# Kernel optimization log

Hardware: AMD Instinct MI355X
Metric: run time of the kernel (lower is better)

The kernel has to match this reference:

```python
import jax, jax.numpy as jnp
import numpy as np

EPS = 1e-12

def gcn_layer(x, W, row, col, vals, n_nodes):
    # support = x @ W ; out = relu(spmm(adj, support)) with adj in COO form
    support = x @ W                                  # [N, out]
    msgs = vals[:, None] * support[col]              # [E, out] gather
    agg = jax.ops.segment_sum(msgs, row, num_segments=n_nodes)
    return jax.nn.relu(agg)

def l2norm(x):
    return x / jnp.maximum(jnp.linalg.norm(x, axis=1, keepdims=True), EPS)

def setup_inputs() -> dict:
    key = jax.random.key(0)
    ks = jax.random.split(key, 16)
    N, D, A, Da, E = 20000, 1000, 1000, 100, 160000
    inp = {
        'emb_sr': jax.random.normal(ks[0], (N, D), jnp.float32) * 0.02,
        'emb_tg': jax.random.normal(ks[1], (N, D), jnp.float32) * 0.02,
        'attr_weight_sr': jax.random.uniform(ks[2], (N, A), jnp.float32),
        'attr_weight_tg': jax.random.uniform(ks[3], (N, A), jnp.float32),
        'row_sr': jax.random.randint(ks[4], (E,), 0, N, jnp.int32),
        'col_sr': jax.random.randint(ks[5], (E,), 0, N, jnp.int32),
        'vals_sr': jax.random.uniform(ks[6], (E,), jnp.float32),
        'row_tg': jax.random.randint(ks[7], (E,), 0, N, jnp.int32),
        'col_tg': jax.random.randint(ks[8], (E,), 0, N, jnp.int32),
        'vals_tg': jax.random.uniform(ks[9], (E,), jnp.float32),
        'W_s0': jax.random.normal(ks[10], (D, D), jnp.float32) * (1.0 / np.sqrt(D)),
        'W_s1': jax.random.normal(ks[11], (D, D), jnp.float32) * (1.0 / np.sqrt(D)),
        'W_a11': jax.random.normal(ks[12], (A, Da), jnp.float32) * (1.0 / np.sqrt(A)),
        'W_a12': jax.random.normal(ks[13], (A, Da), jnp.float32) * (1.0 / np.sqrt(A)),
        'W_a2': jax.random.normal(ks[14], (Da, Da), jnp.float32) * (1.0 / np.sqrt(Da)),
    }
    return inp

def reference(emb_sr, emb_tg, attr_weight_sr, attr_weight_tg,
              row_sr, col_sr, vals_sr, row_tg, col_tg, vals_tg,
              W_s0, W_s1, W_a11, W_a12, W_a2):
    N = emb_sr.shape[0]
    M = emb_tg.shape[0]
    # structural branch: 2 shared GCN layers over each graph
    sr = emb_sr
    tg = emb_tg
    for W in (W_s0, W_s1):
        sr = gcn_layer(sr, W, row_sr, col_sr, vals_sr, N)
        tg = gcn_layer(tg, W, row_tg, col_tg, vals_tg, M)
    sr = l2norm(sr)
    tg = l2norm(tg)
    # attribute branch
    sr_a = gcn_layer(attr_weight_sr, W_a11, row_sr, col_sr, vals_sr, N)
    sr_a = gcn_layer(sr_a, W_a2, row_sr, col_sr, vals_sr, N)
    tg_a = gcn_layer(attr_weight_tg, W_a12, row_tg, col_tg, vals_tg, M)
    tg_a = gcn_layer(tg_a, W_a2, row_tg, col_tg, vals_tg, M)
    return (sr, tg, sr_a, tg_a)
```

## Files before the change

kernel.cpp:

```cpp
#include <hip/hip_runtime.h>

#define N_NODES 20000
#define D_IN    1000
#define E_EDGES 160000
#define DA      100

#define MPAD 20224
#define DP   1024
#define DAP  128
#define MBLK 157
#define NRB  1250
#define PEMAX (E_EDGES + 4 * N_NODES)

typedef __bf16 bf16x8 __attribute__((ext_vector_type(8)));
typedef float  f32x4  __attribute__((ext_vector_type(4)));
typedef short  short8v __attribute__((ext_vector_type(8)));

__device__ __forceinline__ short f2bf(float f) {
  __bf16 h = (__bf16)f;
  return *(short*)&h;
}
__device__ __forceinline__ float bf2f(short s) {
  return __uint_as_float(((unsigned)(unsigned short)s) << 16);
}

#define GLDS16(g, l) __builtin_amdgcn_global_load_lds( \
    (const __attribute__((address_space(1))) void*)(g), \
    (__attribute__((address_space(3))) void*)(l), 16, 0, 0)


__global__ void cvt_pad2_k(const float* __restrict__ s0, const float* __restrict__ s1,
                           int R, int C,
                           short* __restrict__ d0, short* __restrict__ d1, int Cp) {
  const float* src = blockIdx.z ? s1 : s0;
  short* dst = blockIdx.z ? d1 : d0;
  int r = blockIdx.y;
  int c0 = threadIdx.x * 4;
  short4 o = {0, 0, 0, 0};
  if (r < R) {
    if (c0 + 3 < C) {
      float4 v = *(const float4*)&src[(size_t)r * C + c0];
      o.x = f2bf(v.x); o.y = f2bf(v.y); o.z = f2bf(v.z); o.w = f2bf(v.w);
    } else {
#pragma unroll
      for (int j = 0; j < 4; ++j) {
        float v = (c0 + j < C) ? src[(size_t)r * C + c0 + j] : 0.f;
        ((short*)&o)[j] = f2bf(v);
      }
    }
  }
  *(short4*)&dst[(size_t)r * Cp + c0] = o;
}

__global__ void cvt_w_t2_k(const float* __restrict__ s0, const float* __restrict__ s1,
                           int K, int Nc,
                           short* __restrict__ d0, short* __restrict__ d1, int Kp) {
  const float* src = blockIdx.z ? s1 : s0;
  short* dst = blockIdx.z ? d1 : d0;
  int n = blockIdx.y;
  int k = blockIdx.x * blockDim.x + threadIdx.x;
  if (k >= Kp) return;
  float v = (k < K && n < Nc) ? src[(size_t)k * Nc + n] : 0.f;
  dst[(size_t)n * Kp + k] = f2bf(v);
}

__global__ void zero_int_k(int* p, int n) {
  int i = blockIdx.x * blockDim.x + threadIdx.x;
  if (i < n) p[i] = 0;
}


__global__ void hist2_k(const int* __restrict__ row0, const int* __restrict__ row1, int E,
                        int* __restrict__ deg0, int* __restrict__ deg1) {
  int e = blockIdx.x * blockDim.x + threadIdx.x;
  if (e < E) atomicAdd(&deg0[row0[e]], 1);
  else if (e < 2 * E) atomicAdd(&deg1[row1[e - E]], 1);
}

#define SCAN_T 1024
#define SCAN_C 20
__launch_bounds__(SCAN_T)
__global__ void scan_pad2_k(const int* __restrict__ dg0, const int* __restrict__ dg1, int n,
                            int* __restrict__ p0, int* __restrict__ p1) {
  const int* deg = blockIdx.x ? dg1 : dg0;
  int* poffs = blockIdx.x ? p1 : p0;
  __shared__ int lds[SCAN_T];
  int t = threadIdx.x;
  int base = t * SCAN_C;
  int v[SCAN_C];
  int s = 0;
#pragma unroll
  for (int i = 0; i < SCAN_C; ++i) {
    int idx = base + i;
    int x = (idx < n) ? ((deg[idx] + 3) & ~3) : 0;
    s += x;
    v[i] = s;
  }
  lds[t] = s;
  __syncthreads();
  for (int off = 1; off < SCAN_T; off <<= 1) {
    int add = (t >= off) ? lds[t - off] : 0;
    __syncthreads();
    lds[t] += add;
    __syncthreads();
  }
  int prefix = lds[t] - s;
#pragma unroll
  for (int i = 0; i < SCAN_C; ++i) {
    int idx = base + i;
    if (idx < n) poffs[idx + 1] = v[i] + prefix;
  }
  if (t == 0) poffs[0] = 0;
}

__global__ void scatter_pack2_k(const int* __restrict__ row0, const int* __restrict__ col0,
                                const float* __restrict__ val0,
                                const int* __restrict__ row1, const int* __restrict__ col1,
                                const float* __restrict__ val1, int E,
                                const int* __restrict__ po0, const int* __restrict__ po1,
                                int* __restrict__ cur0, int* __restrict__ cur1,
                                int2* __restrict__ pk0, int2* __restrict__ pk1) {
  int e = blockIdx.x * blockDim.x + threadIdx.x;
  if (e < E) {
    int r = row0[e];
    int p = atomicAdd(&cur0[r], 1);
    pk0[po0[r] + p] = make_int2(col0[e], __float_as_int(val0[e]));
  } else if (e < 2 * E) {
    int ee = e - E;
    int r = row1[ee];
    int p = atomicAdd(&cur1[r], 1);
    pk1[po1[r] + p] = make_int2(col1[ee], __float_as_int(val1[ee]));
  }
}

__launch_bounds__(512, 1)
__global__ void gemm8p_k(const short* __restrict__ A0, const short* __restrict__ A1, int lda,
                         const short* __restrict__ Bt0, const short* __restrict__ Bt1, int ldb,
                         short* __restrict__ C0, short* __restrict__ C1, int ldc,
                         int nbCol, int nbRow) {
  __shared__ short lds[8][8192];

  int orig = blockIdx.x;
  int nwg = gridDim.x;
  int q = nwg >> 3, rr = nwg & 7;
  int xcd = orig & 7, idx = orig >> 3;
  int wg = (xcd < rr ? xcd * (q + 1) : rr * (q + 1) + (xcd - rr) * q) + idx;
  int colB = wg % nbCol;
  int t2 = wg / nbCol;
  int rowB = t2 % nbRow;
  int z = t2 / nbRow;

  const short* A  = z ? A1 : A0;
  const short* Bt = z ? Bt1 : Bt0;
  short* C        = z ? C1 : C0;

  const int tid  = threadIdx.x;
  const int lane = tid & 63;
  const int wid  = tid >> 6;
  const int wm   = wid >> 2;
  const int wn   = wid & 3;
  const int rowBase = rowB * 256;
  const int colBase = colB * 256;

  const int sC = (lane & 3) ^ ((lane >> 3) & 3);
  const short* baseA = A  + (size_t)(rowBase + wid * 32 + (lane >> 2)) * lda + sC * 8;
  const short* baseB = Bt + (size_t)(colBase + wid * 32 + (lane >> 2)) * ldb + sC * 8;

  const int chunkR = (lane >> 4) ^ ((lane >> 1) & 3);
  const int offA = (wm * 128 + (lane & 15)) * 32 + chunkR * 8;
  const int offB = (wn * 64  + (lane & 15)) * 32 + chunkR * 8;

  f32x4 acc[8][4];
#pragma unroll
  for (int m = 0; m < 8; ++m)
#pragma unroll
    for (int n = 0; n < 4; ++n)
      acc[m][n] = (f32x4){0.f, 0.f, 0.f, 0.f};

#define STAGE_HALF(h) do { \
    int tt_ = (h) >> 2; \
    int kc_ = tt_ * 64 + (((h) >> 1) & 1) * 32; \
    short* dst_ = &lds[(h) & 7][wid * 1024]; \
    if ((h) & 1) { GLDS16(baseB + kc_, dst_); GLDS16(baseB + kc_ + 16 * ldb, dst_ + 512); } \
    else         { GLDS16(baseA + kc_, dst_); GLDS16(baseA + kc_ + 16 * lda, dst_ + 512); } \
  } while (0)

  STAGE_HALF(0); STAGE_HALF(1); STAGE_HALF(2); STAGE_HALF(3); STAGE_HALF(4);
  asm volatile("s_waitcnt vmcnt(6)" ::: "memory");
  __builtin_amdgcn_s_barrier();
  __builtin_amdgcn_sched_barrier(0);

#define PHASE(P, KS, QM) do { \
    const int sA_ = (4 * t + 2 * (KS)) & 7; \
    const short* pA_ = &lds[sA_][0]; \
    const short* pB_ = &lds[sA_ + 1][0]; \
    bf16x8 af_[4], bv_[4]; \
    _Pragma("unroll") \
    for (int m = 0; m < 4; ++m) af_[m] = *(const bf16x8*)&pA_[offA + ((QM) * 4 + m) * 512]; \
    _Pragma("unroll") \
    for (int n = 0; n < 4; ++n) bv_[n] = *(const bf16x8*)&pB_[offB + n * 512]; \
    { int h_ = 4 * t + (P) + 5; \
      if (h_ < 64) STAGE_HALF(h_); } \
    __builtin_amdgcn_s_barrier(); \
    __builtin_amdgcn_s_setprio(1); \
    _Pragma("unroll") \
    for (int m = 0; m < 4; ++m) \
      _Pragma("unroll") \
      for (int n = 0; n < 4; ++n) \
        acc[(QM) * 4 + m][n] = __builtin_amdgcn_mfma_f32_16x16x32_bf16( \
            af_[m], bv_[n], acc[(QM) * 4 + m][n], 0, 0, 0); \
    __builtin_amdgcn_s_setprio(0); \
    if (t < 14)      { asm volatile("s_waitcnt vmcnt(6)" ::: "memory"); } \
    else if (t == 14) { \
      if ((P) < 3)   { asm volatile("s_waitcnt vmcnt(6)" ::: "memory"); } \
      else           { asm volatile("s_waitcnt vmcnt(4)" ::: "memory"); } \
    } else { \
      if ((P) == 0)  { asm volatile("s_waitcnt vmcnt(2)" ::: "memory"); } \
      else           { asm volatile("s_waitcnt vmcnt(0)" ::: "memory"); } \
    } \
    __builtin_amdgcn_s_barrier(); \
    __builtin_amdgcn_sched_barrier(0); \
  } while (0)

  for (int t = 0; t < 16; ++t) {
    PHASE(0, 0, 0);
    PHASE(1, 0, 1);
    PHASE(2, 1, 0);
    PHASE(3, 1, 1);
  }
#undef PHASE
#undef STAGE_HALF

#pragma unroll
  for (int gm = 0; gm < 8; ++gm) {
#pragma unroll
    for (int n = 0; n < 4; ++n) {
      int r0 = rowBase + wm * 128 + gm * 16 + (lane >> 4) * 4;
      int c  = colBase + wn * 64 + n * 16 + (lane & 15);
#pragma unroll
      for (int reg = 0; reg < 4; ++reg)
        C[(size_t)(r0 + reg) * ldc + c] = f2bf(acc[gm][n][reg]);
    }
  }
}

__launch_bounds__(256, 2)
__global__ void gemm_bf16_k(const short* __restrict__ A0, const short* __restrict__ A1, int lda,
                            const short* __restrict__ Bt0, const short* __restrict__ Bt1, int ldb,
                            short* __restrict__ C0, short* __restrict__ C1, int ldc, int K,
                            int nbCol, int nbRow) {
  __shared__ short As[128 * 64];
  __shared__ short Bs[128 * 64];

  int orig = blockIdx.x;
  int nwg = gridDim.x;
  int q = nwg >> 3, rr = nwg & 7;
  int xcd = orig & 7, idx = orig >> 3;
  int wg = (xcd < rr ? xcd * (q + 1) : rr * (q + 1) + (xcd - rr) * q) + idx;
  int colB = wg % nbCol;
  int t2   = wg / nbCol;
  int rowB = t2 % nbRow;
  int z    = t2 / nbRow;

  const short* A  = z ? A1 : A0;
  const short* Bt = z ? Bt1 : Bt0;
  short* C        = z ? C1 : C0;

  const int tid  = threadIdx.x;
  const int lane = tid & 63;
  const int wid  = tid >> 6;
  const int wr   = wid >> 1;
  const int wc   = wid & 1;
  const int rowBase = rowB * 128;
  const int colBase = colB * 128;

  const int lrow = lane >> 3;
  const int kofs = (lane & 7) * 8;

  f32x4 acc[4][4];
#pragma unroll
  for (int m = 0; m < 4; ++m)
#pragma unroll
    for (int n = 0; n < 4; ++n)
      acc[m][n] = (f32x4){0.f, 0.f, 0.f, 0.f};

  for (int k0 = 0; k0 < K; k0 += 64) {
#pragma unroll
    for (int c = 0; c < 4; ++c) {
      int chunk = wid * 4 + c;
      int r = chunk * 8 + lrow;
      const short* g = A + (size_t)(rowBase + r) * lda + k0 + kofs;
      GLDS16(g, &As[chunk * 8 * 64]);
    }
#pragma unroll
    for (int c = 0; c < 4; ++c) {
      int chunk = wid * 4 + c;
      int r = chunk * 8 + lrow;
      const short* g = Bt + (size_t)(colBase + r) * ldb + k0 + kofs;
      GLDS16(g, &Bs[chunk * 8 * 64]);
    }
    __syncthreads();

    bf16x8 af[2][4], bfr[2][4];
#pragma unroll
    for (int kk = 0; kk < 2; ++kk) {
#pragma unroll
      for (int i = 0; i < 4; ++i) {
        int ar = wr * 64 + i * 16 + (lane & 15);
        af[kk][i]  = *(const bf16x8*)&As[ar * 64 + kk * 32 + (lane >> 4) * 8];
        int br = wc * 64 + i * 16 + (lane & 15);
        bfr[kk][i] = *(const bf16x8*)&Bs[br * 64 + kk * 32 + (lane >> 4) * 8];
      }
    }
#pragma unroll
    for (int kk = 0; kk < 2; ++kk)
#pragma unroll
      for (int m = 0; m < 4; ++m)
#pragma unroll
        for (int n = 0; n < 4; ++n)
          acc[m][n] = __builtin_amdgcn_mfma_f32_16x16x32_bf16(
              af[kk][m], bfr[kk][n], acc[m][n], 0, 0, 0);
    __syncthreads();
  }

#pragma unroll
  for (int m = 0; m < 4; ++m) {
#pragma unroll
    for (int n = 0; n < 4; ++n) {
      int row0 = rowBase + wr * 64 + m * 16 + (lane >> 4) * 4;
      int col  = colBase + wc * 64 + n * 16 + (lane & 15);
#pragma unroll
      for (int reg = 0; reg < 4; ++reg)
        C[(size_t)(row0 + reg) * ldc + col] = f2bf(acc[m][n][reg]);
    }
  }
}

template<int NCHUNK, int MODE>
__launch_bounds__(256)
__global__ void spmm_v5(const int* __restrict__ po0, const int* __restrict__ po1,
                        const int2* __restrict__ pk0, const int2* __restrict__ pk1,
                        const short* __restrict__ S0, const short* __restrict__ S1, int ldS,
                        short* __restrict__ oB0, short* __restrict__ oB1, int ldB,
                        float* __restrict__ oF0, float* __restrict__ oF1, int outCols) {
  int orig = blockIdx.x;
  int chunk, graph, rowBlk;
  if (NCHUNK == 8) {
    chunk = orig & 7;
    int idx = orig >> 3;
    graph = idx / NRB;
    rowBlk = idx - graph * NRB;
  } else {
    chunk = 0;
    graph = orig / NRB;
    rowBlk = orig - graph * NRB;
  }
  const int* poffs   = graph ? po1 : po0;
  const int2* packed = graph ? pk1 : pk0;
  const short* S     = graph ? S1 : S0;
  short* outB        = graph ? oB1 : oB0;
  float* outF        = graph ? oF1 : oF0;

  const int lane16 = threadIdx.x & 15;
  const int rowloc = threadIdx.x >> 4;
  const int r  = rowBlk * 16 + rowloc;
  const int c0 = chunk * 128 + lane16 * 8;

  int e0 = poffs[r], e1 = poffs[r + 1];
  float acc[8];
#pragma unroll
  for (int j = 0; j < 8; ++j) acc[j] = 0.f;

  for (int i = e0; i < e1; i += 4) {
    const int4* p4 = (const int4*)&packed[i];
    int4 a = p4[0];
    int4 b = p4[1];
    short8v s0 = *(const short8v*)&S[(size_t)a.x * ldS + c0];
    short8v s1 = *(const short8v*)&S[(size_t)a.z * ldS + c0];
    short8v s2 = *(const short8v*)&S[(size_t)b.x * ldS + c0];
    short8v s3 = *(const short8v*)&S[(size_t)b.z * ldS + c0];
    float v0 = __int_as_float(a.y);
    float v1 = __int_as_float(a.w);
    float v2 = __int_as_float(b.y);
    float v3 = __int_as_float(b.w);
#pragma unroll
    for (int j = 0; j < 8; ++j) {
      acc[j] += v0 * bf2f(s0[j]);
      acc[j] += v1 * bf2f(s1[j]);
      acc[j] += v2 * bf2f(s2[j]);
      acc[j] += v3 * bf2f(s3[j]);
    }
  }
#pragma unroll
  for (int j = 0; j < 8; ++j) acc[j] = fmaxf(acc[j], 0.f);

  if (MODE == 0) {
    short8v o;
#pragma unroll
    for (int j = 0; j < 8; ++j) o[j] = f2bf(acc[j]);
    *(short8v*)&outB[(size_t)r * ldB + c0] = o;
  } else {
#pragma unroll
    for (int j = 0; j < 8; ++j)
      if (c0 + j < outCols)
        outF[(size_t)r * outCols + c0 + j] = acc[j];
  }
}

__global__ void l2norm2_k(const short* __restrict__ H0, const short* __restrict__ H1, int ldH,
                          float* __restrict__ o0, float* __restrict__ o1, int cols) {
  const short* H = blockIdx.y ? H1 : H0;
  float* out = blockIdx.y ? o1 : o0;
  __shared__ float red[4];
  int r = blockIdx.x;
  int t = threadIdx.x;
  float s = 0.f;
  for (int c = t; c < ldH; c += 256) {
    float v = bf2f(H[(size_t)r * ldH + c]);
    s += v * v;
  }
  for (int off = 32; off >= 1; off >>= 1) s += __shfl_down(s, off, 64);
  if ((t & 63) == 0) red[t >> 6] = s;
  __syncthreads();
  float tot = red[0] + red[1] + red[2] + red[3];
  float inv = 1.f / fmaxf(sqrtf(tot), 1e-12f);
  for (int c = t; c < cols; c += 256)
    out[(size_t)r * cols + c] = bf2f(H[(size_t)r * ldH + c]) * inv;
}


extern "C" void kernel_launch(void* const* d_in, const int* in_sizes, int n_in,
                              void* d_out, int out_size, void* d_ws, size_t ws_size,
                              hipStream_t stream) {
  const float* emb_sr  = (const float*)d_in[0];
  const float* emb_tg  = (const float*)d_in[1];
  const float* attr_sr = (const float*)d_in[2];
  const float* attr_tg = (const float*)d_in[3];
  const int*   row_sr  = (const int*)d_in[4];
  const int*   col_sr  = (const int*)d_in[5];
  const float* vals_sr = (const float*)d_in[6];
  const int*   row_tg  = (const int*)d_in[7];
  const int*   col_tg  = (const int*)d_in[8];
  const float* vals_tg = (const float*)d_in[9];
  const float* W_s0    = (const float*)d_in[10];
  const float* W_s1    = (const float*)d_in[11];
  const float* W_a11   = (const float*)d_in[12];
  const float* W_a12   = (const float*)d_in[13];
  const float* W_a2    = (const float*)d_in[14];

  const int N = N_NODES, Dd = D_IN, E = E_EDGES;

  char* ws = (char*)d_ws;
  size_t off = 0;
  auto alloc = [&](size_t bytes) -> void* {
    void* p = ws + off;
    off += (bytes + 255) & ~(size_t)255;
    return p;
  };
  short* X0 = (short*)alloc((size_t)MPAD * DP * 2);
  short* X1 = (short*)alloc((size_t)MPAD * DP * 2);
  short* T0 = (short*)alloc((size_t)MPAD * DP * 2);
  short* T1 = (short*)alloc((size_t)MPAD * DP * 2);
  short* Ws0t  = (short*)alloc((size_t)DP * DP * 2);
  short* Ws1t  = (short*)alloc((size_t)DP * DP * 2);
  short* Wa11t = (short*)alloc((size_t)DAP * DP * 2);
  short* Wa12t = (short*)alloc((size_t)DAP * DP * 2);
  short* Wa2t  = (short*)alloc((size_t)DAP * DAP * 2);
  int*  ibuf    = (int*)alloc((size_t)4 * N * 4);
  int2* pack_sr = (int2*)alloc((size_t)PEMAX * 8);
  int2* pack_tg = (int2*)alloc((size_t)PEMAX * 8);
  int*  poffs_sr = (int*)alloc((size_t)(N + 1) * 4);
  int*  poffs_tg = (int*)alloc((size_t)(N + 1) * 4);
  if (off > ws_size) return;

  int* deg_sr = ibuf;
  int* cur_sr = ibuf + N;
  int* deg_tg = ibuf + 2 * N;
  int* cur_tg = ibuf + 3 * N;
  const int ZERO_N = 4 * N + 2 * (PEMAX * 2);

  float* out_sr  = (float*)d_out;
  float* out_tg  = out_sr + (size_t)N * Dd;
  float* out_sra = out_tg + (size_t)N * Dd;
  float* out_tga = out_sra + (size_t)N * DA;

  zero_int_k<<<dim3((ZERO_N + 255) / 256), 256, 0, stream>>>(ibuf, ZERO_N);
  hist2_k<<<dim3((2 * E + 255) / 256), 256, 0, stream>>>(row_sr, row_tg, E, deg_sr, deg_tg);
  scan_pad2_k<<<2, SCAN_T, 0, stream>>>(deg_sr, deg_tg, N, poffs_sr, poffs_tg);
  scatter_pack2_k<<<dim3((2 * E + 255) / 256), 256, 0, stream>>>(
      row_sr, col_sr, vals_sr, row_tg, col_tg, vals_tg, E,
      poffs_sr, poffs_tg, cur_sr, cur_tg, pack_sr, pack_tg);

  cvt_w_t2_k<<<dim3(DP / 256, DP, 2), 256, 0, stream>>>(W_s0, W_s1, Dd, Dd, Ws0t, Ws1t, DP);
  cvt_w_t2_k<<<dim3(DP / 256, DAP, 2), 256, 0, stream>>>(W_a11, W_a12, Dd, DA, Wa11t, Wa12t, DP);
  cvt_w_t2_k<<<dim3(1, DAP, 1), 256, 0, stream>>>(W_a2, W_a2, DA, DA, Wa2t, Wa2t, DAP);

  cvt_pad2_k<<<dim3(1, MPAD, 2), 256, 0, stream>>>(emb_sr, emb_tg, N, Dd, X0, X1, DP);
  gemm8p_k<<<dim3(79 * 4 * 2), 512, 0, stream>>>(X0, X1, DP, Ws0t, Ws0t, DP,
                                                 T0, T1, DP, 4, 79);
  spmm_v5<8, 0><<<dim3(8 * 2 * NRB), 256, 0, stream>>>(
      poffs_sr, poffs_tg, pack_sr, pack_tg, T0, T1, DP, X0, X1, DP, nullptr, nullptr, 0);
  gemm8p_k<<<dim3(79 * 4 * 2), 512, 0, stream>>>(X0, X1, DP, Ws1t, Ws1t, DP,
                                                 T0, T1, DP, 4, 79);
  spmm_v5<8, 0><<<dim3(8 * 2 * NRB), 256, 0, stream>>>(
      poffs_sr, poffs_tg, pack_sr, pack_tg, T0, T1, DP, X0, X1, DP, nullptr, nullptr, 0);
  l2norm2_k<<<dim3(N, 2), 256, 0, stream>>>(X0, X1, DP, out_sr, out_tg, Dd);

  cvt_pad2_k<<<dim3(1, MPAD, 2), 256, 0, stream>>>(attr_sr, attr_tg, N, Dd, X0, X1, DP);
  gemm_bf16_k<<<dim3(1 * MBLK * 2), 256, 0, stream>>>(X0, X1, DP, Wa11t, Wa12t, DP,
                                                      T0, T1, DAP, DP, 1, MBLK);
  spmm_v5<1, 0><<<dim3(2 * NRB), 256, 0, stream>>>(
      poffs_sr, poffs_tg, pack_sr, pack_tg, T0, T1, DAP, X0, X1, DAP, nullptr, nullptr, 0);
  gemm_bf16_k<<<dim3(1 * MBLK * 2), 256, 0, stream>>>(X0, X1, DAP, Wa2t, Wa2t, DAP,
                                                      T0, T1, DAP, DAP, 1, MBLK);
  spmm_v5<1, 1><<<dim3(2 * NRB), 256, 0, stream>>>(
      poffs_sr, poffs_tg, pack_sr, pack_tg, T0, T1, DAP, nullptr, nullptr, 0, out_sra, out_tga, DA);
}
```

Baseline: 636.9 us.

## Restructure GEMM inner phases, merge input conversions, vectorize l2norm

The gemm8p main loop is unrolled by hand into four explicit phases. The B fragments are loaded once per K-substep and reused across both M halves, and the barrier/waitcnt placement is changed so that only alternate phases wait on global loads. The two fp32→bf16 pad conversions become one launch that writes into separate Y buffers for the attribute inputs, which removes one launch at the cost of extra workspace. l2norm reads each row once as short4 and keeps the values in registers, avoiding a second pass over global memory. The reduced waitcnt/barrier structure risks subtle races if the LDS ring slots are overwritten early.

```diff
diff --git a/kernel.cpp b/kernel.cpp
--- a/kernel.cpp
+++ b/kernel.cpp
@@ -29,11 +29,18 @@
     (__attribute__((address_space(3))) void*)(l), 16, 0, 0)
 
 
-__global__ void cvt_pad2_k(const float* __restrict__ s0, const float* __restrict__ s1,
+__global__ void cvt_pad4_k(const float* __restrict__ s0, const float* __restrict__ s1,
+                           const float* __restrict__ s2, const float* __restrict__ s3,
                            int R, int C,
-                           short* __restrict__ d0, short* __restrict__ d1, int Cp) {
-  const float* src = blockIdx.z ? s1 : s0;
-  short* dst = blockIdx.z ? d1 : d0;
+                           short* __restrict__ d0, short* __restrict__ d1,
+                           short* __restrict__ d2, short* __restrict__ d3, int Cp) {
+  const float* src; short* dst;
+  switch (blockIdx.z) {
+    case 0:  src = s0; dst = d0; break;
+    case 1:  src = s1; dst = d1; break;
+    case 2:  src = s2; dst = d2; break;
+    default: src = s3; dst = d3; break;
+  }
   int r = blockIdx.y;
   int c0 = threadIdx.x * 4;
   short4 o = {0, 0, 0, 0};
@@ -188,47 +195,87 @@
   STAGE_HALF(0); STAGE_HALF(1); STAGE_HALF(2); STAGE_HALF(3); STAGE_HALF(4);
   asm volatile("s_waitcnt vmcnt(6)" ::: "memory");
   __builtin_amdgcn_s_barrier();
-  __builtin_amdgcn_sched_barrier(0);
-
-#define PHASE(P, KS, QM) do { \
-    const int sA_ = (4 * t + 2 * (KS)) & 7; \
-    const short* pA_ = &lds[sA_][0]; \
-    const short* pB_ = &lds[sA_ + 1][0]; \
-    bf16x8 af_[4], bv_[4]; \
-    _Pragma("unroll") \
-    for (int m = 0; m < 4; ++m) af_[m] = *(const bf16x8*)&pA_[offA + ((QM) * 4 + m) * 512]; \
-    _Pragma("unroll") \
-    for (int n = 0; n < 4; ++n) bv_[n] = *(const bf16x8*)&pB_[offB + n * 512]; \
-    { int h_ = 4 * t + (P) + 5; \
-      if (h_ < 64) STAGE_HALF(h_); } \
-    __builtin_amdgcn_s_barrier(); \
-    __builtin_amdgcn_s_setprio(1); \
-    _Pragma("unroll") \
-    for (int m = 0; m < 4; ++m) \
-      _Pragma("unroll") \
-      for (int n = 0; n < 4; ++n) \
-        acc[(QM) * 4 + m][n] = __builtin_amdgcn_mfma_f32_16x16x32_bf16( \
-            af_[m], bv_[n], acc[(QM) * 4 + m][n], 0, 0, 0); \
-    __builtin_amdgcn_s_setprio(0); \
-    if (t < 14)      { asm volatile("s_waitcnt vmcnt(6)" ::: "memory"); } \
-    else if (t == 14) { \
-      if ((P) < 3)   { asm volatile("s_waitcnt vmcnt(6)" ::: "memory"); } \
-      else           { asm volatile("s_waitcnt vmcnt(4)" ::: "memory"); } \
-    } else { \
-      if ((P) == 0)  { asm volatile("s_waitcnt vmcnt(2)" ::: "memory"); } \
-      else           { asm volatile("s_waitcnt vmcnt(0)" ::: "memory"); } \
-    } \
-    __builtin_amdgcn_s_barrier(); \
-    __builtin_amdgcn_sched_barrier(0); \
-  } while (0)
-
+
+  bf16x8 bv[4];
   for (int t = 0; t < 16; ++t) {
-    PHASE(0, 0, 0);
-    PHASE(1, 0, 1);
-    PHASE(2, 1, 0);
-    PHASE(3, 1, 1);
-  }
-#undef PHASE
+    const int s0 = (4 * t) & 7;
+    const int s1 = (4 * t + 2) & 7;
+
+    {
+      const short* pA = &lds[s0][0];
+      const short* pB = &lds[s0 + 1][0];
+      bf16x8 af[4];
+#pragma unroll
+      for (int n = 0; n < 4; ++n) bv[n] = *(const bf16x8*)&pB[offB + n * 512];
+#pragma unroll
+      for (int m = 0; m < 4; ++m) af[m] = *(const bf16x8*)&pA[offA + m * 512];
+      { int h = 4 * t + 5; if (h < 64) STAGE_HALF(h); }
+      __builtin_amdgcn_s_barrier();
+      __builtin_amdgcn_s_setprio(1);
+#pragma unroll
+      for (int m = 0; m < 4; ++m)
+#pragma unroll
+        for (int n = 0; n < 4; ++n)
+          acc[m][n] = __builtin_amdgcn_mfma_f32_16x16x32_bf16(af[m], bv[n], acc[m][n], 0, 0, 0);
+      __builtin_amdgcn_s_setprio(0);
+      __builtin_amdgcn_s_barrier();
+    }
+    {
+      const short* pA = &lds[s0][0];
+      bf16x8 af[4];
+#pragma unroll
+      for (int m = 0; m < 4; ++m) af[m] = *(const bf16x8*)&pA[offA + (4 + m) * 512];
+      { int h = 4 * t + 6; if (h < 64) STAGE_HALF(h); }
+      __builtin_amdgcn_s_barrier();
+      __builtin_amdgcn_s_setprio(1);
+#pragma unroll
+      for (int m = 0; m < 4; ++m)
+#pragma unroll
+        for (int n = 0; n < 4; ++n)
+          acc[4 + m][n] = __builtin_amdgcn_mfma_f32_16x16x32_bf16(af[m], bv[n], acc[4 + m][n], 0, 0, 0);
+      __builtin_amdgcn_s_setprio(0);
+      if (t < 15) { asm volatile("s_waitcnt vmcnt(6)" ::: "memory"); }
+      else        { asm volatile("s_waitcnt vmcnt(0)" ::: "memory"); }
+      __builtin_amdgcn_s_barrier();
+    }
+    {
+      const short* pA = &lds[s1][0];
+      const short* pB = &lds[s1 + 1][0];
+      bf16x8 af[4];
+#pragma unroll
+      for (int n = 0; n < 4; ++n) bv[n] = *(const bf16x8*)&pB[offB + n * 512];
+#pragma unroll
+      for (int m = 0; m < 4; ++m) af[m] = *(const bf16x8*)&pA[offA + m * 512];
+      { int h = 4 * t + 7; if (h < 64) STAGE_HALF(h); }
+      __builtin_amdgcn_s_barrier();
+      __builtin_amdgcn_s_setprio(1);
+#pragma unroll
+      for (int m = 0; m < 4; ++m)
+#pragma unroll
+        for (int n = 0; n < 4; ++n)
+          acc[m][n] = __builtin_amdgcn_mfma_f32_16x16x32_bf16(af[m], bv[n], acc[m][n], 0, 0, 0);
+      __builtin_amdgcn_s_setprio(0);
+      __builtin_amdgcn_s_barrier();
+    }
+    {
+      const short* pA = &lds[s1][0];
+      bf16x8 af[4];
+#pragma unroll
+      for (int m = 0; m < 4; ++m) af[m] = *(const bf16x8*)&pA[offA + (4 + m) * 512];
+      { int h = 4 * t + 8; if (h < 64) STAGE_HALF(h); }
+      __builtin_amdgcn_s_barrier();
+      __builtin_amdgcn_s_setprio(1);
+#pragma unroll
+      for (int m = 0; m < 4; ++m)
+#pragma unroll
+        for (int n = 0; n < 4; ++n)
+          acc[4 + m][n] = __builtin_amdgcn_mfma_f32_16x16x32_bf16(af[m], bv[n], acc[4 + m][n], 0, 0, 0);
+      __builtin_amdgcn_s_setprio(0);
+      if (t < 14)       { asm volatile("s_waitcnt vmcnt(6)" ::: "memory"); }
+      else if (t == 14) { asm volatile("s_waitcnt vmcnt(4)" ::: "memory"); }
+      __builtin_amdgcn_s_barrier();
+    }
+  }
 #undef STAGE_HALF
 
 #pragma unroll
@@ -407,6 +454,7 @@
   }
 }
 
+__launch_bounds__(256)
 __global__ void l2norm2_k(const short* __restrict__ H0, const short* __restrict__ H1, int ldH,
                           float* __restrict__ o0, float* __restrict__ o1, int cols) {
   const short* H = blockIdx.y ? H1 : H0;
@@ -414,18 +462,20 @@
   __shared__ float red[4];
   int r = blockIdx.x;
   int t = threadIdx.x;
-  float s = 0.f;
-  for (int c = t; c < ldH; c += 256) {
-    float v = bf2f(H[(size_t)r * ldH + c]);
-    s += v * v;
-  }
+  short4 v = ((const short4*)(H + (size_t)r * ldH))[t];
+  float f0 = bf2f(v.x), f1 = bf2f(v.y), f2 = bf2f(v.z), f3 = bf2f(v.w);
+  float s = f0 * f0 + f1 * f1 + f2 * f2 + f3 * f3;
   for (int off = 32; off >= 1; off >>= 1) s += __shfl_down(s, off, 64);
   if ((t & 63) == 0) red[t >> 6] = s;
   __syncthreads();
   float tot = red[0] + red[1] + red[2] + red[3];
   float inv = 1.f / fmaxf(sqrtf(tot), 1e-12f);
-  for (int c = t; c < cols; c += 256)
-    out[(size_t)r * cols + c] = bf2f(H[(size_t)r * ldH + c]) * inv;
+  int c0 = t * 4;
+  float vals[4] = {f0, f1, f2, f3};
+#pragma unroll
+  for (int j = 0; j < 4; ++j)
+    if (c0 + j < cols)
+      out[(size_t)r * cols + c0 + j] = vals[j] * inv;
 }
 
 
@@ -461,6 +511,8 @@
   short* X1 = (short*)alloc((size_t)MPAD * DP * 2);
   short* T0 = (short*)alloc((size_t)MPAD * DP * 2);
   short* T1 = (short*)alloc((size_t)MPAD * DP * 2);
+  short* Y0 = (short*)alloc((size_t)MPAD * DP * 2);
+  short* Y1 = (short*)alloc((size_t)MPAD * DP * 2);
   short* Ws0t  = (short*)alloc((size_t)DP * DP * 2);
   short* Ws1t  = (short*)alloc((size_t)DP * DP * 2);
   short* Wa11t = (short*)alloc((size_t)DAP * DP * 2);
@@ -491,11 +543,12 @@
       row_sr, col_sr, vals_sr, row_tg, col_tg, vals_tg, E,
       poffs_sr, poffs_tg, cur_sr, cur_tg, pack_sr, pack_tg);
 
+  cvt_pad4_k<<<dim3(1, MPAD, 4), 256, 0, stream>>>(emb_sr, emb_tg, attr_sr, attr_tg,
+                                                   N, Dd, X0, X1, Y0, Y1, DP);
   cvt_w_t2_k<<<dim3(DP / 256, DP, 2), 256, 0, stream>>>(W_s0, W_s1, Dd, Dd, Ws0t, Ws1t, DP);
   cvt_w_t2_k<<<dim3(DP / 256, DAP, 2), 256, 0, stream>>>(W_a11, W_a12, Dd, DA, Wa11t, Wa12t, DP);
   cvt_w_t2_k<<<dim3(1, DAP, 1), 256, 0, stream>>>(W_a2, W_a2, DA, DA, Wa2t, Wa2t, DAP);
 
-  cvt_pad2_k<<<dim3(1, MPAD, 2), 256, 0, stream>>>(emb_sr, emb_tg, N, Dd, X0, X1, DP);
   gemm8p_k<<<dim3(79 * 4 * 2), 512, 0, stream>>>(X0, X1, DP, Ws0t, Ws0t, DP,
                                                  T0, T1, DP, 4, 79);
   spmm_v5<8, 0><<<dim3(8 * 2 * NRB), 256, 0, stream>>>(
@@ -506,8 +559,7 @@
       poffs_sr, poffs_tg, pack_sr, pack_tg, T0, T1, DP, X0, X1, DP, nullptr, nullptr, 0);
   l2norm2_k<<<dim3(N, 2), 256, 0, stream>>>(X0, X1, DP, out_sr, out_tg, Dd);
 
-  cvt_pad2_k<<<dim3(1, MPAD, 2), 256, 0, stream>>>(attr_sr, attr_tg, N, Dd, X0, X1, DP);
-  gemm_bf16_k<<<dim3(1 * MBLK * 2), 256, 0, stream>>>(X0, X1, DP, Wa11t, Wa12t, DP,
+  gemm_bf16_k<<<dim3(1 * MBLK * 2), 256, 0, stream>>>(Y0, Y1, DP, Wa11t, Wa12t, DP,
                                                       T0, T1, DAP, DP, 1, MBLK);
   spmm_v5<1, 0><<<dim3(2 * NRB), 256, 0, stream>>>(
       poffs_sr, poffs_tg, pack_sr, pack_tg, T0, T1, DAP, X0, X1, DAP, nullptr, nullptr, 0);
```

New measurement: 634.2 us, median of 2. No clear change (-0.4%).
